# Kernel tuning notes

Measured on AMD Instinct MI355X. Metric: run time of the kernel, lower is better.

Reference implementation:

```python
import jax, jax.numpy as jnp
import numpy as np

EMBED_DIM = 1024
NUM_HEADS = 16
HEAD_DIM = EMBED_DIM // NUM_HEADS


def setup_inputs() -> dict:
    key = jax.random.key(0)
    k_x, k_wqkv, k_bqkv, k_wo, k_bo = jax.random.split(key, 5)
    B, T, C = 4, 2048, EMBED_DIM
    s_in = 1.0 / np.sqrt(C)
    return {
        "x": jax.random.normal(k_x, (B, T, C), dtype=jnp.float32),
        # torch Linear: weight [out,in]; we store transposed [in,out] for x @ W
        "w_qkv": jax.random.uniform(k_wqkv, (C, 3 * C), dtype=jnp.float32, minval=-s_in, maxval=s_in),
        "b_qkv": jax.random.uniform(k_bqkv, (3 * C,), dtype=jnp.float32, minval=-s_in, maxval=s_in),
        "w_out": jax.random.uniform(k_wo, (C, C), dtype=jnp.float32, minval=-s_in, maxval=s_in),
        "b_out": jax.random.uniform(k_bo, (C,), dtype=jnp.float32, minval=-s_in, maxval=s_in),
    }


def reference(x, w_qkv, b_qkv, w_out, b_out):
    B, T, C = x.shape
    H, D = NUM_HEADS, HEAD_DIM
    qkv = x @ w_qkv + b_qkv                       # [B,T,3C]
    qkv = qkv.reshape(B, T, 3, H, D)
    q, k, v = qkv[:, :, 0], qkv[:, :, 1], qkv[:, :, 2]   # [B,T,H,D]
    q = q.transpose(0, 2, 1, 3)                   # [B,H,T,D]
    k = k.transpose(0, 2, 1, 3)
    v = v.transpose(0, 2, 1, 3)
    scale = 1.0 / np.sqrt(D).astype(np.float32)
    att = jnp.einsum("bhqd,bhkd->bhqk", q, k) * scale   # [B,H,T,T]
    causal = jnp.tril(jnp.ones((T, T), dtype=bool))
    att = jnp.where(causal[None, None], att, -jnp.inf)
    att = jax.nn.softmax(att, axis=-1)
    y = jnp.einsum("bhqk,bhkd->bhqd", att, v)     # [B,H,T,D]
    y = y.transpose(0, 2, 1, 3).reshape(B, T, C)
    return y @ w_out + b_out
```

## Files before the change

kernel.cpp:

```cpp
#include <hip/hip_runtime.h>
#include <hip/hip_bf16.h>

#define EMBED 1024
#define NHEAD 16
#define HDIM  64
#define BATCH 4
#define SEQ   2048
#define BT    (BATCH*SEQ)
#define NQKV  (3*EMBED)

using bf16x8 = __attribute__((ext_vector_type(8))) short;
using f32x4  = __attribute__((ext_vector_type(4))) float;

__device__ __forceinline__ unsigned short f2bf(float f){
  union { float f; unsigned u; } v; v.f = f;
  unsigned r = v.u + 0x7FFFu + ((v.u >> 16) & 1u);
  return (unsigned short)(r >> 16);
}

__device__ __forceinline__ float exp2_hw(float x){
  float r; asm("v_exp_f32 %0, %1" : "=v"(r) : "v"(x)); return r;
}
__device__ __forceinline__ unsigned cvtpk_bf16(float lo, float hi){
  unsigned r; asm("v_cvt_pk_bf16_f32 %0, %1, %2" : "=v"(r) : "v"(lo), "v"(hi));
  return r;
}

__device__ __forceinline__ void gload_lds16(const void* g, void* l){
  __builtin_amdgcn_global_load_lds(
      (const __attribute__((address_space(1))) void*)g,
      (__attribute__((address_space(3))) void*)l, 16, 0, 0);
}

__global__ __launch_bounds__(256) void cvt_f32_bf16_k(
    const float* __restrict__ in, unsigned short* __restrict__ out, int n)
{
  int i = (blockIdx.x * 256 + threadIdx.x) * 4;
  if (i >= n) return;
  float4 v = *(const float4*)&in[i];
  ushort4 o;
  o.x = f2bf(v.x); o.y = f2bf(v.y); o.z = f2bf(v.z); o.w = f2bf(v.w);
  *(ushort4*)&out[i] = o;
}

__global__ __launch_bounds__(256) void transpose_cvt_k(
    const float* __restrict__ in, unsigned short* __restrict__ out, int R, int C)
{
  __shared__ float tile[32][33];
  int tx = threadIdx.x, ty = threadIdx.y;
  int c0 = blockIdx.x * 32, r0 = blockIdx.y * 32;
#pragma unroll
  for (int j = ty; j < 32; j += 8)
    tile[j][tx] = in[(size_t)(r0 + j) * C + c0 + tx];
  __syncthreads();
#pragma unroll
  for (int j = ty; j < 32; j += 8)
    out[(size_t)(c0 + j) * R + r0 + tx] = f2bf(tile[tx][j]);
}

template<int EPI>
__global__ __launch_bounds__(256) void gemm_bt(
    const unsigned short* __restrict__ A,
    const unsigned short* __restrict__ Bt,
    const float* __restrict__ bias,
    unsigned short* __restrict__ qp,
    unsigned short* __restrict__ kp,
    unsigned short* __restrict__ vp,
    float* __restrict__ outp,
    int M, int N, int K)
{
  __shared__ unsigned short As[128 * 64];
  __shared__ unsigned short Bs[128 * 64];
  const int tid = threadIdx.x;
  const int w = tid >> 6, lane = tid & 63;
  const int lr = lane & 15, lg = lane >> 4;
  const int gy = gridDim.y;
  const int lin = (int)(blockIdx.y * gridDim.x + blockIdx.x);
  const int cpx = (int)(gridDim.x * gy) >> 3;
  const int wg = (lin & 7) * cpx + (lin >> 3);
  const int m0 = (wg / gy) * 128, n0 = (wg % gy) * 128;
  const int wm = (w >> 1) * 64, wn = (w & 1) * 64;
  const int fbase = w * 4;
  f32x4 acc[4][4] = {};

  for (int kt = 0; kt < K; kt += 64) {
    __syncthreads();
#pragma unroll
    for (int i = 0; i < 4; i++) {
      int f = (fbase + i) * 64 + lane;
      int row = f >> 3, col = (f & 7) * 8;
      gload_lds16(A  + (size_t)(m0 + row) * K + kt + col, &As[(fbase + i) * 512]);
      gload_lds16(Bt + (size_t)(n0 + row) * K + kt + col, &Bs[(fbase + i) * 512]);
    }
    __syncthreads();
#pragma unroll
    for (int kk = 0; kk < 2; kk++) {
      bf16x8 af[4], bv[4];
#pragma unroll
      for (int mi = 0; mi < 4; mi++)
        af[mi] = *(const bf16x8*)&As[(wm + mi * 16 + lr) * 64 + kk * 32 + lg * 8];
#pragma unroll
      for (int ni = 0; ni < 4; ni++)
        bv[ni] = *(const bf16x8*)&Bs[(wn + ni * 16 + lr) * 64 + kk * 32 + lg * 8];
#pragma unroll
      for (int mi = 0; mi < 4; mi++)
#pragma unroll
        for (int ni = 0; ni < 4; ni++)
          acc[mi][ni] = __builtin_amdgcn_mfma_f32_16x16x32_bf16(af[mi], bv[ni], acc[mi][ni], 0, 0, 0);
    }
  }

#pragma unroll
  for (int mi = 0; mi < 4; mi++)
#pragma unroll
    for (int ni = 0; ni < 4; ni++) {
      const int rowb = m0 + wm + mi * 16 + lg * 4;
      const int colb = n0 + wn + ni * 16 + lr;
      const float bv_ = bias[colb];
      if (EPI == 0) {
        int s = colb >> 10, hh = (colb & 1023) >> 6, d = colb & 63;
        int b = rowb >> 11, t = rowb & 2047;
        if (s == 2) {
          ushort4 o4;
          o4.x = f2bf(acc[mi][ni][0] + bv_);
          o4.y = f2bf(acc[mi][ni][1] + bv_);
          o4.z = f2bf(acc[mi][ni][2] + bv_);
          o4.w = f2bf(acc[mi][ni][3] + bv_);
          *(ushort4*)&vp[((size_t)(b * NHEAD + hh) * HDIM + d) * SEQ + t] = o4;
        } else {
          unsigned short* dst = (s == 0) ? qp : kp;
          const float scl = (s == 0) ? 0.18033688f : 1.0f;
#pragma unroll
          for (int r = 0; r < 4; r++)
            dst[((size_t)(b * NHEAD + hh) * SEQ + t + r) * HDIM + d] =
                f2bf((acc[mi][ni][r] + bv_) * scl);
        }
      } else {
#pragma unroll
        for (int r = 0; r < 4; r++)
          outp[(size_t)(rowb + r) * N + colb] = acc[mi][ni][r] + bv_;
      }
    }
}

__device__ __forceinline__ void softmax_frag(
    f32x4 (&s)[4], float& m, f32x4& su, f32x4 (&o)[4],
    unsigned short* psrow, int qrow, int kbase, bool needmask,
    int lg, int lr, int pswz)
{
  const float NEG = -1e30f;
  if (needmask) {
#pragma unroll
    for (int n = 0; n < 4; n++)
#pragma unroll
      for (int r = 0; r < 4; r++) {
        if (kbase + n * 16 + lg * 4 + r > qrow) s[n][r] = NEG;
      }
  }
  float t0 = fmaxf(fmaxf(s[0][0], s[0][1]), fmaxf(s[0][2], s[0][3]));
  float t1 = fmaxf(fmaxf(s[1][0], s[1][1]), fmaxf(s[1][2], s[1][3]));
  float t2 = fmaxf(fmaxf(s[2][0], s[2][1]), fmaxf(s[2][2], s[2][3]));
  float t3 = fmaxf(fmaxf(s[3][0], s[3][1]), fmaxf(s[3][2], s[3][3]));
  float pm = fmaxf(fmaxf(t0, t1), fmaxf(t2, t3));
  if (__any(pm > m + 8.f)) {
    pm = fmaxf(pm, __shfl_xor(pm, 16, 64));
    pm = fmaxf(pm, __shfl_xor(pm, 32, 64));
    float mn = fmaxf(m, pm);
    float fac = exp2_hw(m - mn);
    m = mn;
    float fr[4];
#pragma unroll
    for (int r = 0; r < 4; r++) fr[r] = __shfl(fac, lg * 4 + r, 64);
#pragma unroll
    for (int r = 0; r < 4; r++) su[r] *= fr[r];
#pragma unroll
    for (int n = 0; n < 4; n++)
#pragma unroll
      for (int r = 0; r < 4; r++) o[n][r] *= fr[r];
  }
#pragma unroll
  for (int n = 0; n < 4; n++) {
    float p0 = exp2_hw(s[n][0] - m);
    float p1 = exp2_hw(s[n][1] - m);
    float p2 = exp2_hw(s[n][2] - m);
    float p3 = exp2_hw(s[n][3] - m);
    uint2 pk;
    pk.x = cvtpk_bf16(p0, p1);
    pk.y = cvtpk_bf16(p2, p3);
    int E = (lr * 64 + n * 16 + lg * 4) ^ pswz;
    *(uint2*)&psrow[E] = pk;
  }
}

__global__ __launch_bounds__(256) void attn_k(
    const unsigned short* __restrict__ Q,
    const unsigned short* __restrict__ K,
    const unsigned short* __restrict__ Vt,
    unsigned short* __restrict__ Y)
{
  __shared__ unsigned short Ks[2][64 * 64];
  __shared__ unsigned short Vs[2][64 * 64];
  __shared__ unsigned short Ps[4][32 * 64];

  const int tid = threadIdx.x;
  const int w = tid >> 6, lane = tid & 63;
  const int lr = lane & 15, lg = lane >> 4;
  const int bh = blockIdx.y;
  const int b = bh >> 4, h = bh & 15;
  const size_t base = (size_t)bh * SEQ * HDIM;
  const float NEG = -1e30f;
  const int pswz = (lr & 7) << 3;

  bf16x8 ones;
#pragma unroll
  for (int e = 0; e < 8; e++) ones[e] = (short)0x3F80;

  const int f0 = w * 128 + lane, f1 = f0 + 64;
  const int r0_ = f0 >> 3, c0_ = ((f0 & 7) ^ (r0_ & 7)) * 8;
  const int r1_ = f1 >> 3, c1_ = ((f1 & 7) ^ (r1_ & 7)) * 8;

  for (int seg = 0; seg < 2; seg++) {
    const int qb = seg ? (int)blockIdx.x : (15 - (int)blockIdx.x);
    const int qw0 = qb * 128 + w * 32;
    const int nk = 2 * qb + 2;

    bf16x8 aq[2][2];
#pragma unroll
    for (int f = 0; f < 2; f++)
#pragma unroll
      for (int kk = 0; kk < 2; kk++)
        aq[f][kk] = *(const bf16x8*)
            &Q[base + (size_t)(qw0 + f * 16 + lr) * HDIM + kk * 32 + lg * 8];

    f32x4 o0[4] = {}, o1[4] = {};
    f32x4 su0 = {}, su1 = {};
    float m0 = NEG, m1 = NEG;

    {
      const unsigned short* kxp = K + base;
      const unsigned short* vxp = Vt + base;
      gload_lds16(kxp + r0_ * HDIM + c0_, &Ks[0][f0 * 8]);
      gload_lds16(kxp + r1_ * HDIM + c1_, &Ks[0][f1 * 8]);
      gload_lds16(vxp + (size_t)r0_ * SEQ + c0_, &Vs[0][f0 * 8]);
      gload_lds16(vxp + (size_t)r1_ * SEQ + c1_, &Vs[0][f1 * 8]);
    }
    __syncthreads();

    int cur = 0;
    for (int kb = 0; kb < nk; kb++) {
      if (kb + 1 < nk) {
        const unsigned short* kxp = K + base + (size_t)(kb + 1) * 64 * HDIM;
        const unsigned short* vxp = Vt + base + (kb + 1) * 64;
        gload_lds16(kxp + r0_ * HDIM + c0_, &Ks[cur ^ 1][f0 * 8]);
        gload_lds16(kxp + r1_ * HDIM + c1_, &Ks[cur ^ 1][f1 * 8]);
        gload_lds16(vxp + (size_t)r0_ * SEQ + c0_, &Vs[cur ^ 1][f0 * 8]);
        gload_lds16(vxp + (size_t)r1_ * SEQ + c1_, &Vs[cur ^ 1][f1 * 8]);
      }

      const bool active = (kb * 64 <= qw0 + 31);
      if (active) {
        f32x4 s0[4] = {}, s1[4] = {};
        __builtin_amdgcn_s_setprio(1);
#pragma unroll
        for (int kk = 0; kk < 2; kk++) {
          bf16x8 bk[4];
#pragma unroll
          for (int n = 0; n < 4; n++) {
            int E = (n * 16 + lr) * 64 + kk * 32 + lg * 8;
            bk[n] = *(const bf16x8*)&Ks[cur][E ^ pswz];
          }
#pragma unroll
          for (int n = 0; n < 4; n++) {
            s0[n] = __builtin_amdgcn_mfma_f32_16x16x32_bf16(bk[n], aq[0][kk], s0[n], 0, 0, 0);
            s1[n] = __builtin_amdgcn_mfma_f32_16x16x32_bf16(bk[n], aq[1][kk], s1[n], 0, 0, 0);
          }
        }
        __builtin_amdgcn_s_setprio(0);

        const int kbase = kb * 64;
        softmax_frag(s0, m0, su0, o0, &Ps[w][0],
                     qw0 + lr, kbase, kbase + 63 > qw0, lg, lr, pswz);
        softmax_frag(s1, m1, su1, o1, &Ps[w][16 * 64],
                     qw0 + 16 + lr, kbase, kbase + 63 > qw0 + 16, lg, lr, pswz);

        __builtin_amdgcn_s_setprio(1);
#pragma unroll
        for (int kc = 0; kc < 2; kc++) {
          bf16x8 ap0 = *(const bf16x8*)&Ps[w][(lr * 64 + kc * 32 + lg * 8) ^ pswz];
          bf16x8 ap1 = *(const bf16x8*)&Ps[w][((16 + lr) * 64 + kc * 32 + lg * 8) ^ pswz];
          su0 = __builtin_amdgcn_mfma_f32_16x16x32_bf16(ap0, ones, su0, 0, 0, 0);
          su1 = __builtin_amdgcn_mfma_f32_16x16x32_bf16(ap1, ones, su1, 0, 0, 0);
#pragma unroll
          for (int n = 0; n < 4; n++) {
            int E = (n * 16 + lr) * 64 + kc * 32 + lg * 8;
            bf16x8 bv = *(const bf16x8*)&Vs[cur][E ^ pswz];
            o0[n] = __builtin_amdgcn_mfma_f32_16x16x32_bf16(ap0, bv, o0[n], 0, 0, 0);
            o1[n] = __builtin_amdgcn_mfma_f32_16x16x32_bf16(ap1, bv, o1[n], 0, 0, 0);
          }
        }
        __builtin_amdgcn_s_setprio(0);
      }

      __syncthreads();
      cur ^= 1;
    }

    float inv0[4], inv1[4];
#pragma unroll
    for (int r = 0; r < 4; r++) { inv0[r] = 1.f / su0[r]; inv1[r] = 1.f / su1[r]; }
#pragma unroll
    for (int n = 0; n < 4; n++)
#pragma unroll
      for (int r = 0; r < 4; r++) {
        int col = h * HDIM + n * 16 + lr;
        int t0 = qw0 + lg * 4 + r;
        Y[((size_t)(b * SEQ + t0)) * EMBED + col] = f2bf(o0[n][r] * inv0[r]);
        int t1 = qw0 + 16 + lg * 4 + r;
        Y[((size_t)(b * SEQ + t1)) * EMBED + col] = f2bf(o1[n][r] * inv1[r]);
      }
  }
}

extern "C" void kernel_launch(void* const* d_in, const int* in_sizes, int n_in,
                              void* d_out, int out_size, void* d_ws, size_t ws_size,
                              hipStream_t stream) {
  const float* x     = (const float*)d_in[0];
  const float* w_qkv = (const float*)d_in[1];
  const float* b_qkv = (const float*)d_in[2];
  const float* w_out = (const float*)d_in[3];
  const float* b_out = (const float*)d_in[4];
  float* outp = (float*)d_out;

  char* ws = (char*)d_ws;
  unsigned short* xb    = (unsigned short*)ws; ws += (size_t)BT * EMBED * 2;
  unsigned short* wqkvT = (unsigned short*)ws; ws += (size_t)NQKV * EMBED * 2;
  unsigned short* woutT = (unsigned short*)ws; ws += (size_t)EMBED * EMBED * 2;
  unsigned short* Qb    = (unsigned short*)ws; ws += (size_t)BATCH * NHEAD * SEQ * HDIM * 2;
  unsigned short* Kb    = (unsigned short*)ws; ws += (size_t)BATCH * NHEAD * SEQ * HDIM * 2;
  unsigned short* Vb    = (unsigned short*)ws; ws += (size_t)BATCH * NHEAD * SEQ * HDIM * 2;
  unsigned short* Yb    = (unsigned short*)ws; ws += (size_t)BT * EMBED * 2;

  cvt_f32_bf16_k<<<(BT * EMBED) / 1024, 256, 0, stream>>>(x, xb, BT * EMBED);
  transpose_cvt_k<<<dim3(NQKV / 32, EMBED / 32), dim3(32, 8), 0, stream>>>(w_qkv, wqkvT, EMBED, NQKV);
  transpose_cvt_k<<<dim3(EMBED / 32, EMBED / 32), dim3(32, 8), 0, stream>>>(w_out, woutT, EMBED, EMBED);

  gemm_bt<0><<<dim3(BT / 128, NQKV / 128), 256, 0, stream>>>(
      xb, wqkvT, b_qkv, Qb, Kb, Vb, nullptr, BT, NQKV, EMBED);

  attn_k<<<dim3(8, BATCH * NHEAD), 256, 0, stream>>>(Qb, Kb, Vb, Yb);

  gemm_bt<1><<<dim3(BT / 128, EMBED / 128), 256, 0, stream>>>(
      Yb, woutT, b_out, nullptr, nullptr, nullptr, outp, BT, EMBED, EMBED);
}
```

Baseline: 209.4 us.

## Double-buffer LDS tiles in GEMM to overlap global loads with MFMA

The GEMM main loop now uses two LDS buffers per operand. The next K-tile is prefetched with direct-to-LDS loads while MFMAs run on the current tile, which cuts one of the two barriers per iteration. It also raises wave priority around the MFMA block. This doubles LDS use per block to 64KB, which may reduce occupancy.

Result: faster. 202.2 us (-3.4%).

```diff
diff --git a/kernel.cpp b/kernel.cpp
--- a/kernel.cpp
+++ b/kernel.cpp
@@ -69,8 +69,8 @@
     float* __restrict__ outp,
     int M, int N, int K)
 {
-  __shared__ unsigned short As[128 * 64];
-  __shared__ unsigned short Bs[128 * 64];
+  __shared__ unsigned short As[2][128 * 64];
+  __shared__ unsigned short Bs[2][128 * 64];
   const int tid = threadIdx.x;
   const int w = tid >> 6, lane = tid & 63;
   const int lr = lane & 15, lg = lane >> 4;
@@ -83,31 +83,56 @@
   const int fbase = w * 4;
   f32x4 acc[4][4] = {};
 
-  for (int kt = 0; kt < K; kt += 64) {
-    __syncthreads();
-#pragma unroll
-    for (int i = 0; i < 4; i++) {
-      int f = (fbase + i) * 64 + lane;
-      int row = f >> 3, col = (f & 7) * 8;
-      gload_lds16(A  + (size_t)(m0 + row) * K + kt + col, &As[(fbase + i) * 512]);
-      gload_lds16(Bt + (size_t)(n0 + row) * K + kt + col, &Bs[(fbase + i) * 512]);
-    }
-    __syncthreads();
+  int srow[4], scol[4];
+#pragma unroll
+  for (int i = 0; i < 4; i++) {
+    int f = (fbase + i) * 64 + lane;
+    srow[i] = f >> 3;
+    scol[i] = (f & 7) * 8;
+  }
+
+  const int nkt = K >> 6;
+
+#pragma unroll
+  for (int i = 0; i < 4; i++) {
+    gload_lds16(A  + (size_t)(m0 + srow[i]) * K + scol[i], &As[0][(fbase + i) * 512]);
+    gload_lds16(Bt + (size_t)(n0 + srow[i]) * K + scol[i], &Bs[0][(fbase + i) * 512]);
+  }
+  __syncthreads();
+
+  int cur = 0;
+  for (int t = 0; t < nkt; t++) {
+    if (t + 1 < nkt) {
+      const int kt = (t + 1) << 6;
+#pragma unroll
+      for (int i = 0; i < 4; i++) {
+        gload_lds16(A  + (size_t)(m0 + srow[i]) * K + kt + scol[i],
+                    &As[cur ^ 1][(fbase + i) * 512]);
+        gload_lds16(Bt + (size_t)(n0 + srow[i]) * K + kt + scol[i],
+                    &Bs[cur ^ 1][(fbase + i) * 512]);
+      }
+    }
+
 #pragma unroll
     for (int kk = 0; kk < 2; kk++) {
       bf16x8 af[4], bv[4];
 #pragma unroll
       for (int mi = 0; mi < 4; mi++)
-        af[mi] = *(const bf16x8*)&As[(wm + mi * 16 + lr) * 64 + kk * 32 + lg * 8];
+        af[mi] = *(const bf16x8*)&As[cur][(wm + mi * 16 + lr) * 64 + kk * 32 + lg * 8];
 #pragma unroll
       for (int ni = 0; ni < 4; ni++)
-        bv[ni] = *(const bf16x8*)&Bs[(wn + ni * 16 + lr) * 64 + kk * 32 + lg * 8];
+        bv[ni] = *(const bf16x8*)&Bs[cur][(wn + ni * 16 + lr) * 64 + kk * 32 + lg * 8];
+      __builtin_amdgcn_s_setprio(1);
 #pragma unroll
       for (int mi = 0; mi < 4; mi++)
 #pragma unroll
         for (int ni = 0; ni < 4; ni++)
           acc[mi][ni] = __builtin_amdgcn_mfma_f32_16x16x32_bf16(af[mi], bv[ni], acc[mi][ni], 0, 0, 0);
-    }
+      __builtin_amdgcn_s_setprio(0);
+    }
+
+    __syncthreads();
+    cur ^= 1;
   }
 
 #pragma unroll
```
